# Performance work log

Measured on AMD Instinct MI355X. Metric: run time of the kernel, lower is better.

The kernel has to match this reference:

```python
import jax, jax.numpy as jnp
import numpy as np

B, S, D = 2, 2048, 1024
H = 16
HD = D // H  # 64


def _rope_tables(seq_len, head_dim, dtype=jnp.float32):
    inv_freq = 1.0 / (10000.0 ** (jnp.arange(0, head_dim, 2, dtype=jnp.float32) / head_dim))
    t = jnp.arange(seq_len, dtype=jnp.float32)
    freqs = jnp.einsum('i,j->ij', t, inv_freq)            # [S, HD/2]
    emb = jnp.concatenate([freqs, freqs], axis=-1)        # [S, HD]
    return jnp.cos(emb).astype(dtype)[None, None], jnp.sin(emb).astype(dtype)[None, None]


def _rotate_half(x):
    x1, x2 = x[..., : x.shape[-1] // 2], x[..., x.shape[-1] // 2 :]
    return jnp.concatenate([-x2, x1], axis=-1)


def setup_inputs() -> dict:
    key = jax.random.key(0)
    ks = jax.random.split(key, 9)
    s = 0.02
    return {
        'hidden_states': jax.random.normal(ks[0], (B, S, D), jnp.float32),
        'attention_mask': jnp.zeros((B, 1, S, S), jnp.float32),
        'Wq': jax.random.normal(ks[1], (D, D), jnp.float32) * s,
        'bq': jnp.zeros((D,), jnp.float32),
        'Wk': jax.random.normal(ks[2], (D, D), jnp.float32) * s,
        'bk': jnp.zeros((D,), jnp.float32),
        'Wv': jax.random.normal(ks[3], (D, D), jnp.float32) * s,
        'bv': jnp.zeros((D,), jnp.float32),
        'Wo': jax.random.normal(ks[4], (D, D), jnp.float32) * s,
        'bo': jnp.zeros((D,), jnp.float32),
    }


def reference(hidden_states, attention_mask, Wq, bq, Wk, bk, Wv, bv, Wo, bo):
    b, s = hidden_states.shape[:2]
    q = hidden_states @ Wq.T + bq
    k = hidden_states @ Wk.T + bk
    v = hidden_states @ Wv.T + bv
    # [B, H, S, HD]
    q = q.reshape(b, s, H, HD).transpose(0, 2, 1, 3)
    k = k.reshape(b, s, H, HD).transpose(0, 2, 1, 3)
    v = v.reshape(b, s, H, HD).transpose(0, 2, 1, 3)
    cos, sin = _rope_tables(s, HD, q.dtype)
    q = q * cos + _rotate_half(q) * sin
    k = k * cos + _rotate_half(k) * sin
    scaling = HD ** (-0.5)
    scores = jnp.einsum('bhqd,bhkd->bhqk', q, k) * scaling
    scores = scores / jnp.log(jnp.asarray(float(s), scores.dtype))  # dynamic NTK
    scores = scores + attention_mask
    probs = jax.nn.softmax(scores, axis=-1)
    out = jnp.einsum('bhqk,bhkd->bhqd', probs, v)
    out = out.transpose(0, 2, 1, 3).reshape(b, s, H * HD)
    return out @ Wo.T + bo
```

## Files before the change

### kernel.cpp

```cpp
#include <hip/hip_runtime.h>
#include <math.h>

#define S_LEN 2048
#define NHEAD 16
#define HDIM  64

typedef __attribute__((ext_vector_type(8))) short bf16x8;
typedef __attribute__((ext_vector_type(4))) float f32x4;

__device__ __forceinline__ unsigned short f2bf(float f) {
    union { float f; unsigned u; } v; v.f = f;
    unsigned r = v.u + 0x7fffu + ((v.u >> 16) & 1u);
    return (unsigned short)(r >> 16);
}

__device__ __forceinline__ void gl2lds16(const void* g, void* l) {
    __builtin_amdgcn_global_load_lds(
        (__attribute__((address_space(1))) void*)(void*)(g),
        (__attribute__((address_space(3))) void*)(l), 16, 0, 0);
}

__global__ __launch_bounds__(256) void convert_kernel(
    const float* __restrict__ hs, const float* __restrict__ Wq,
    const float* __restrict__ Wk, const float* __restrict__ Wv,
    const float* __restrict__ Wo, unsigned short* __restrict__ dst,
    float2* __restrict__ rtab)
{
    const int bid = blockIdx.x;
    if (bid >= 8192) {
        const int gid = (bid - 8192) * 256 + threadIdx.x;
        const int s = gid >> 5, i = gid & 31;
        const float l2c = 0.41524101186092029f;
        const float freq = exp2f(-(float)i * l2c);
        const float ang = (float)s * freq;
        float2 cs;
        cs.x = cosf(ang);
        cs.y = sinf(ang);
        rtab[gid] = cs;
        return;
    }
    const int gid = bid * 256 + threadIdx.x;
    const int n = gid << 2;
    const float* src; int off;
    if (n < (4 << 20))      { src = hs; off = n; }
    else if (n < (5 << 20)) { src = Wq; off = n - (4 << 20); }
    else if (n < (6 << 20)) { src = Wk; off = n - (5 << 20); }
    else if (n < (7 << 20)) { src = Wv; off = n - (6 << 20); }
    else                    { src = Wo; off = n - (7 << 20); }
    const float4 v = *(const float4*)(src + off);
    ushort4 o;
    o.x = f2bf(v.x); o.y = f2bf(v.y); o.z = f2bf(v.z); o.w = f2bf(v.w);
    *(ushort4*)(dst + n) = o;
}

__global__ __launch_bounds__(256, 3) void qkv_gemm_kernel(
    const unsigned short* __restrict__ X,
    const unsigned short* __restrict__ Wall,
    const float* __restrict__ bq, const float* __restrict__ bk,
    const float* __restrict__ bv, const float2* __restrict__ rtab,
    unsigned short* __restrict__ qo, unsigned short* __restrict__ ko,
    unsigned short* __restrict__ vo)
{
    __shared__ unsigned short As[128 * 64];
    __shared__ unsigned short Bs[128 * 64];

    const int mat = blockIdx.x >> 3;
    const int n0  = (blockIdx.x & 7) << 7;
    const int m0  = blockIdx.y << 7;
    const unsigned short* W = Wall + (mat << 20);
    const float* bias = (mat == 0) ? bq : (mat == 1) ? bk : bv;
    unsigned short* out = (mat == 0) ? qo : (mat == 1) ? ko : vo;

    const int tid = threadIdx.x;
    const int wave = tid >> 6, lane = tid & 63;
    const int quad = lane >> 4, ln = lane & 15;
    const int wm = (wave >> 1) << 6, wn = (wave & 1) << 6;

    const unsigned short* xptr[4];
    const unsigned short* wptr[4];
    #pragma unroll
    for (int L = 0; L < 4; ++L) {
        const int i = tid + (L << 8);
        const int r = i >> 3, cl = i & 7;
        const int cg = (cl ^ (r & 7)) << 3;
        const int rq = r & 63;
        const int tau = (mat < 2)
            ? ((r & 64) | ((rq & 15) << 1) | ((rq >> 4) & 1) | (((rq >> 5) & 1) << 5))
            : ((r & 64) | ((rq & 15) << 2) | (rq >> 4));
        xptr[L] = X + (m0 + r) * 1024 + cg;
        wptr[L] = W + (n0 + tau) * 1024 + cg;
    }

    f32x4 acc[4][4] = {};

    for (int k0 = 0; k0 < 1024; k0 += 64) {
        #pragma unroll
        for (int L = 0; L < 4; ++L) {
            const int i = tid + (L << 8);
            gl2lds16(xptr[L] + k0, &As[i << 3]);
            gl2lds16(wptr[L] + k0, &Bs[i << 3]);
        }
        __syncthreads();
        #pragma unroll
        for (int s = 0; s < 2; ++s) {
            bf16x8 a[4], b[4];
            #pragma unroll
            for (int t = 0; t < 4; ++t) {
                const int ra = wm + (t << 4) + ln;
                a[t] = *(const bf16x8*)&As[(ra << 6) + ((((s << 2) | quad) ^ (ra & 7)) << 3)];
                const int rb = wn + (t << 4) + ln;
                b[t] = *(const bf16x8*)&Bs[(rb << 6) + ((((s << 2) | quad) ^ (rb & 7)) << 3)];
            }
            #pragma unroll
            for (int i = 0; i < 4; ++i)
                #pragma unroll
                for (int j = 0; j < 4; ++j)
                    acc[i][j] = __builtin_amdgcn_mfma_f32_16x16x32_bf16(a[i], b[j], acc[i][j], 0, 0, 0);
        }
        __syncthreads();
    }

    const int h = (n0 + wn) >> 6;

    if (mat < 2) {
        const int nb = n0 + wn + (ln << 1);
        const float b0 = bias[nb],      b1 = bias[nb + 1];
        const float b2 = bias[nb + 32], b3 = bias[nb + 33];
        #pragma unroll
        for (int i = 0; i < 4; ++i) {
            #pragma unroll
            for (int reg = 0; reg < 4; ++reg) {
                const int m = m0 + wm + (i << 4) + (quad << 2) + reg;
                const int b_ = m >> 11, s_ = m & 2047;
                unsigned short* o = out + ((((b_ << 4) + h) << 11) + s_) * 64;
                const float4 cs = *(const float4*)(rtab + (s_ << 5) + (ln << 1));
                const float x1a = acc[i][0][reg] + b0, x1b = acc[i][1][reg] + b1;
                const float x2a = acc[i][2][reg] + b2, x2b = acc[i][3][reg] + b3;
                const float r0a = x1a * cs.x - x2a * cs.y;
                const float r0b = x1b * cs.z - x2b * cs.w;
                const float r1a = x2a * cs.x + x1a * cs.y;
                const float r1b = x2b * cs.z + x1b * cs.w;
                const unsigned ua = __float_as_uint(r0a) + 0x8000u;
                const unsigned ub = __float_as_uint(r0b) + 0x8000u;
                const unsigned uc = __float_as_uint(r1a) + 0x8000u;
                const unsigned ud = __float_as_uint(r1b) + 0x8000u;
                *(unsigned*)(o + (ln << 1))      = __builtin_amdgcn_perm(ub, ua, 0x07060302u);
                *(unsigned*)(o + 32 + (ln << 1)) = __builtin_amdgcn_perm(ud, uc, 0x07060302u);
            }
        }
    } else {
        const float4 bv4 = *(const float4*)(bias + n0 + wn + (ln << 2));
        #pragma unroll
        for (int i = 0; i < 4; ++i)
            #pragma unroll
            for (int reg = 0; reg < 4; ++reg) {
                const int m = m0 + wm + (i << 4) + (quad << 2) + reg;
                const int b_ = m >> 11, s_ = m & 2047;
                unsigned short* o = out + ((((b_ << 4) + h) << 11) + s_) * 64;
                const unsigned ua = __float_as_uint(acc[i][0][reg] + bv4.x) + 0x8000u;
                const unsigned ub = __float_as_uint(acc[i][1][reg] + bv4.y) + 0x8000u;
                const unsigned uc = __float_as_uint(acc[i][2][reg] + bv4.z) + 0x8000u;
                const unsigned ud = __float_as_uint(acc[i][3][reg] + bv4.w) + 0x8000u;
                uint2 w;
                w.x = __builtin_amdgcn_perm(ub, ua, 0x07060302u);
                w.y = __builtin_amdgcn_perm(ud, uc, 0x07060302u);
                *(uint2*)(o + (ln << 2)) = w;
            }
    }
}

__global__ __launch_bounds__(256) void vtrans_kernel(
    const unsigned short* __restrict__ v, unsigned short* __restrict__ vt)
{
    __shared__ unsigned short T[64][66];
    const int bh = blockIdx.x >> 5;
    const int s0 = (blockIdx.x & 31) << 6;
    const int tid = threadIdx.x;
    #pragma unroll
    for (int L = 0; L < 4; ++L) {
        const int i = tid + (L << 8);
        const int r = i >> 4, c4 = (i & 15) << 2;
        const ushort4 in = *(const ushort4*)(v + ((bh << 11) + s0 + r) * 64 + c4);
        T[r][c4 + 0] = in.x; T[r][c4 + 1] = in.y;
        T[r][c4 + 2] = in.z; T[r][c4 + 3] = in.w;
    }
    __syncthreads();
    #pragma unroll
    for (int L = 0; L < 4; ++L) {
        const int i = tid + (L << 8);
        const int hd = i >> 4, c4 = (i & 15) << 2;
        ushort4 o;
        o.x = T[c4 + 0][hd]; o.y = T[c4 + 1][hd];
        o.z = T[c4 + 2][hd]; o.w = T[c4 + 3][hd];
        *(ushort4*)(vt + ((bh << 6) + hd) * 2048 + s0 + c4) = o;
    }
}

__global__ __launch_bounds__(256, 4) void flash_kernel(
    const unsigned short* __restrict__ qb, const unsigned short* __restrict__ kb,
    const unsigned short* __restrict__ vtb, const float* __restrict__ mask,
    unsigned short* __restrict__ attn)
{
    __shared__ unsigned short Ks[2][64 * 64];
    __shared__ unsigned short Vt[2][64 * 64];
    __shared__ unsigned short Ps[64 * 64];

    const int qt = blockIdx.x & 31;
    const int bh = blockIdx.x >> 5;
    const int b_ = bh >> 4, h = bh & 15;
    const int q0 = qt << 6;

    const int tid = threadIdx.x;
    const int wave = tid >> 6, lane = tid & 63;
    const int quad = lane >> 4, ln = lane & 15;

    const unsigned short* qrow = qb + ((size_t)((bh << 11) + q0 + (wave << 4) + ln) << 6);
    bf16x8 qa[2];
    qa[0] = *(const bf16x8*)(qrow + (quad << 3));
    qa[1] = *(const bf16x8*)(qrow + 32 + (quad << 3));

    const float scale = 0.125f / logf(2048.0f);

    const float* mbase = mask + ((size_t)b_ << 22)
                       + ((size_t)(q0 + (wave << 4) + (quad << 2)) << 11) + (ln << 2);

    unsigned short* Pw = Ps + (wave << 10);

    const int i0 = tid, i1 = tid + 256;
    const int r0 = i0 >> 3, c0 = ((i0 & 7) ^ (r0 & 7)) << 3;
    const int r1 = i1 >> 3, c1 = ((i1 & 7) ^ (r1 & 7)) << 3;
    const int p0 = ((r0 & 15) << 2) + (r0 >> 4);
    const int p1 = ((r1 & 15) << 2) + (r1 >> 4);
    const unsigned short* kg0 = kb + ((bh << 11) + p0) * 64 + c0;
    const unsigned short* kg1 = kb + ((bh << 11) + p1) * 64 + c1;
    const unsigned short* vg0 = vtb + ((bh << 6) + r0) * 2048 + c0;
    const unsigned short* vg1 = vtb + ((bh << 6) + r1) * 2048 + c1;

    float l_i[4] = {0.f, 0.f, 0.f, 0.f};
    f32x4 O[4] = {};

    gl2lds16(kg0, &Ks[0][i0 << 3]);
    gl2lds16(kg1, &Ks[0][i1 << 3]);
    gl2lds16(vg0, &Vt[0][i0 << 3]);
    gl2lds16(vg1, &Vt[0][i1 << 3]);
    float4 mcur[4];
    #pragma unroll
    for (int reg = 0; reg < 4; ++reg)
        mcur[reg] = *(const float4*)(mbase + (reg << 11));

    for (int kt = 0; kt < 32; ++kt) {
        const int cur = kt & 1;

        __syncthreads();

        float4 mnext[4];
        if (kt < 31) {
            const int kn = (kt + 1) << 6;
            gl2lds16(kg0 + (kn << 6), &Ks[cur ^ 1][i0 << 3]);
            gl2lds16(kg1 + (kn << 6), &Ks[cur ^ 1][i1 << 3]);
            gl2lds16(vg0 + kn, &Vt[cur ^ 1][i0 << 3]);
            gl2lds16(vg1 + kn, &Vt[cur ^ 1][i1 << 3]);
            #pragma unroll
            for (int reg = 0; reg < 4; ++reg)
                mnext[reg] = *(const float4*)(mbase + kn + (reg << 11));
        }

        f32x4 sacc[4] = {};
        #pragma unroll
        for (int s = 0; s < 2; ++s) {
            bf16x8 bfr[4];
            #pragma unroll
            for (int j = 0; j < 4; ++j) {
                const int r = (j << 4) + ln;
                bfr[j] = *(const bf16x8*)&Ks[cur][(r << 6) + ((((s << 2) | quad) ^ (r & 7)) << 3)];
            }
            #pragma unroll
            for (int j = 0; j < 4; ++j)
                sacc[j] = __builtin_amdgcn_mfma_f32_16x16x32_bf16(qa[s], bfr[j], sacc[j], 0, 0, 0);
        }

        #pragma unroll
        for (int reg = 0; reg < 4; ++reg) {
            const int pr = (quad << 2) + reg;
            const float m0f = mcur[reg].x, m1f = mcur[reg].y,
                        m2f = mcur[reg].z, m3f = mcur[reg].w;
            float p[4];
            p[0] = __expf(fmaf(sacc[0][reg], scale, m0f));
            p[1] = __expf(fmaf(sacc[1][reg], scale, m1f));
            p[2] = __expf(fmaf(sacc[2][reg], scale, m2f));
            p[3] = __expf(fmaf(sacc[3][reg], scale, m3f));
            l_i[reg] += (p[0] + p[1]) + (p[2] + p[3]);
            unsigned u0 = __float_as_uint(p[0]) + 0x8000u;
            unsigned u1 = __float_as_uint(p[1]) + 0x8000u;
            unsigned u2 = __float_as_uint(p[2]) + 0x8000u;
            unsigned u3 = __float_as_uint(p[3]) + 0x8000u;
            uint2 w;
            w.x = __builtin_amdgcn_perm(u1, u0, 0x07060302u);
            w.y = __builtin_amdgcn_perm(u3, u2, 0x07060302u);
            const int e = (pr << 6) + ((((ln >> 1) ^ (pr & 7)) << 3)) + ((ln & 1) << 2);
            *(uint2*)&Pw[e] = w;
        }

        #pragma unroll
        for (int s = 0; s < 2; ++s) {
            const bf16x8 a = *(const bf16x8*)&Pw[(ln << 6) + ((((s << 2) | quad) ^ (ln & 7)) << 3)];
            bf16x8 bfr[4];
            #pragma unroll
            for (int j = 0; j < 4; ++j) {
                const int r = (j << 4) + ln;
                bfr[j] = *(const bf16x8*)&Vt[cur][(r << 6) + ((((s << 2) | quad) ^ (r & 7)) << 3)];
            }
            #pragma unroll
            for (int j = 0; j < 4; ++j)
                O[j] = __builtin_amdgcn_mfma_f32_16x16x32_bf16(a, bfr[j], O[j], 0, 0, 0);
        }

        if (kt < 31) {
            #pragma unroll
            for (int reg = 0; reg < 4; ++reg)
                mcur[reg] = mnext[reg];
        }
    }

    #pragma unroll
    for (int reg = 0; reg < 4; ++reg) {
        float l = l_i[reg];
        l += __shfl_xor(l, 1);
        l += __shfl_xor(l, 2);
        l += __shfl_xor(l, 4);
        l += __shfl_xor(l, 8);
        const float inv = 1.0f / l;
        const int qr = q0 + (wave << 4) + (quad << 2) + reg;
        unsigned short* op = attn + (((size_t)((b_ << 11) + qr)) << 10) + (h << 6);
        #pragma unroll
        for (int j = 0; j < 4; ++j)
            op[(j << 4) + ln] = f2bf(O[j][reg] * inv);
    }
}

__global__ __launch_bounds__(256, 3) void out_gemm_kernel(
    const unsigned short* __restrict__ X, const unsigned short* __restrict__ W,
    const float* __restrict__ bias, float* __restrict__ out)
{
    __shared__ unsigned short As[128 * 64];
    __shared__ unsigned short Bs[128 * 64];

    const int n0 = blockIdx.x << 7;
    const int m0 = blockIdx.y << 7;
    const int tid = threadIdx.x;
    const int wave = tid >> 6, lane = tid & 63;
    const int quad = lane >> 4, ln = lane & 15;
    const int wm = (wave >> 1) << 6, wn = (wave & 1) << 6;

    const unsigned short* xptr[4];
    const unsigned short* wptr[4];
    #pragma unroll
    for (int L = 0; L < 4; ++L) {
        const int i = tid + (L << 8);
        const int r = i >> 3, cl = i & 7;
        const int cg = (cl ^ (r & 7)) << 3;
        const int rq = r & 63;
        const int tau = (r & 64) | ((rq & 15) << 2) | (rq >> 4);
        xptr[L] = X + (m0 + r) * 1024 + cg;
        wptr[L] = W + (n0 + tau) * 1024 + cg;
    }

    f32x4 acc[4][4] = {};

    for (int k0 = 0; k0 < 1024; k0 += 64) {
        #pragma unroll
        for (int L = 0; L < 4; ++L) {
            const int i = tid + (L << 8);
            gl2lds16(xptr[L] + k0, &As[i << 3]);
            gl2lds16(wptr[L] + k0, &Bs[i << 3]);
        }
        __syncthreads();
        #pragma unroll
        for (int s = 0; s < 2; ++s) {
            bf16x8 a[4], b[4];
            #pragma unroll
            for (int t = 0; t < 4; ++t) {
                const int ra = wm + (t << 4) + ln;
                a[t] = *(const bf16x8*)&As[(ra << 6) + ((((s << 2) | quad) ^ (ra & 7)) << 3)];
                const int rb = wn + (t << 4) + ln;
                b[t] = *(const bf16x8*)&Bs[(rb << 6) + ((((s << 2) | quad) ^ (rb & 7)) << 3)];
            }
            #pragma unroll
            for (int i = 0; i < 4; ++i)
                #pragma unroll
                for (int j = 0; j < 4; ++j)
                    acc[i][j] = __builtin_amdgcn_mfma_f32_16x16x32_bf16(a[i], b[j], acc[i][j], 0, 0, 0);
        }
        __syncthreads();
    }

    const float4 bv4 = *(const float4*)(bias + n0 + wn + (ln << 2));

    #pragma unroll
    for (int i = 0; i < 4; ++i)
        #pragma unroll
        for (int reg = 0; reg < 4; ++reg) {
            const int m = m0 + wm + (i << 4) + (quad << 2) + reg;
            float4 ov;
            ov.x = acc[i][0][reg] + bv4.x;
            ov.y = acc[i][1][reg] + bv4.y;
            ov.z = acc[i][2][reg] + bv4.z;
            ov.w = acc[i][3][reg] + bv4.w;
            *(float4*)(out + m * 1024 + n0 + wn + (ln << 2)) = ov;
        }
}

extern "C" void kernel_launch(void* const* d_in, const int* in_sizes, int n_in,
                              void* d_out, int out_size, void* d_ws, size_t ws_size,
                              hipStream_t stream)
{
    const float* hs   = (const float*)d_in[0];
    const float* mask = (const float*)d_in[1];
    const float* Wq   = (const float*)d_in[2];
    const float* bq   = (const float*)d_in[3];
    const float* Wk   = (const float*)d_in[4];
    const float* bk   = (const float*)d_in[5];
    const float* Wv   = (const float*)d_in[6];
    const float* bv   = (const float*)d_in[7];
    const float* Wo   = (const float*)d_in[8];
    const float* bo   = (const float*)d_in[9];

    unsigned short* ws = (unsigned short*)d_ws;
    const size_t M1 = (size_t)1 << 20;
    unsigned short* hsb   = ws;
    unsigned short* wall  = ws + 4 * M1;
    unsigned short* wob   = ws + 7 * M1;
    unsigned short* qbf   = ws + 8 * M1;
    unsigned short* kbf   = ws + 12 * M1;
    unsigned short* vbf   = ws + 16 * M1;
    unsigned short* vtb   = ws + 20 * M1;
    unsigned short* attnb = ws + 24 * M1;
    float2*         rtab  = (float2*)(ws + 28 * M1);

    convert_kernel<<<8448, 256, 0, stream>>>(hs, Wq, Wk, Wv, Wo, ws, rtab);
    qkv_gemm_kernel<<<dim3(24, 32), 256, 0, stream>>>(hsb, wall, bq, bk, bv, rtab, qbf, kbf, vbf);
    vtrans_kernel<<<1024, 256, 0, stream>>>(vbf, vtb);
    flash_kernel<<<1024, 256, 0, stream>>>(qbf, kbf, vtb, mask, attnb);
    out_gemm_kernel<<<dim3(8, 32), 256, 0, stream>>>(attnb, wob, bo, (float*)d_out);
}
```

Measured before the change: 225.2 us.

## Fuse V transpose into QKV GEMM epilogue and software-pipeline PV in flash

The QKV GEMM epilogue for V now writes directly in transposed [bh, hd, s] layout, which removes the separate vtrans kernel launch and its extra global round trip. The flash kernel double-buffers the P tile in shared memory and defers each tile's P·V MFMA to the start of the next iteration, so it can overlap with the QK work, with a final PV step after the loop. In exchange, shared memory use grows and the launch bound drops to 3 blocks per CU, which may lower occupancy. The transposed V stores are 8-byte strided writes, which may coalesce less well.

```diff
diff --git a/kernel.cpp b/kernel.cpp
--- a/kernel.cpp
+++ b/kernel.cpp
@@ -59,7 +59,7 @@
     const float* __restrict__ bq, const float* __restrict__ bk,
     const float* __restrict__ bv, const float2* __restrict__ rtab,
     unsigned short* __restrict__ qo, unsigned short* __restrict__ ko,
-    unsigned short* __restrict__ vo)
+    unsigned short* __restrict__ vt)
 {
     __shared__ unsigned short As[128 * 64];
     __shared__ unsigned short Bs[128 * 64];
@@ -69,7 +69,6 @@
     const int m0  = blockIdx.y << 7;
     const unsigned short* W = Wall + (mat << 20);
     const float* bias = (mat == 0) ? bq : (mat == 1) ? bk : bv;
-    unsigned short* out = (mat == 0) ? qo : (mat == 1) ? ko : vo;
 
     const int tid = threadIdx.x;
     const int wave = tid >> 6, lane = tid & 63;
@@ -123,6 +122,7 @@
     const int h = (n0 + wn) >> 6;
 
     if (mat < 2) {
+        unsigned short* out = (mat == 0) ? qo : ko;
         const int nb = n0 + wn + (ln << 1);
         const float b0 = bias[nb],      b1 = bias[nb + 1];
         const float b2 = bias[nb + 32], b3 = bias[nb + 33];
@@ -150,60 +150,36 @@
         }
     } else {
         const float4 bv4 = *(const float4*)(bias + n0 + wn + (ln << 2));
-        #pragma unroll
-        for (int i = 0; i < 4; ++i)
-            #pragma unroll
-            for (int reg = 0; reg < 4; ++reg) {
-                const int m = m0 + wm + (i << 4) + (quad << 2) + reg;
-                const int b_ = m >> 11, s_ = m & 2047;
-                unsigned short* o = out + ((((b_ << 4) + h) << 11) + s_) * 64;
-                const unsigned ua = __float_as_uint(acc[i][0][reg] + bv4.x) + 0x8000u;
-                const unsigned ub = __float_as_uint(acc[i][1][reg] + bv4.y) + 0x8000u;
-                const unsigned uc = __float_as_uint(acc[i][2][reg] + bv4.z) + 0x8000u;
-                const unsigned ud = __float_as_uint(acc[i][3][reg] + bv4.w) + 0x8000u;
+        const float bvv[4] = {bv4.x, bv4.y, bv4.z, bv4.w};
+        #pragma unroll
+        for (int i = 0; i < 4; ++i) {
+            const int m = m0 + wm + (i << 4) + (quad << 2);
+            const int b_ = m >> 11, s_ = m & 2047;
+            const int bh = (b_ << 4) + h;
+            #pragma unroll
+            for (int jt = 0; jt < 4; ++jt) {
+                const int hd = (ln << 2) + jt;
+                const unsigned ua = __float_as_uint(acc[i][jt][0] + bvv[jt]) + 0x8000u;
+                const unsigned ub = __float_as_uint(acc[i][jt][1] + bvv[jt]) + 0x8000u;
+                const unsigned uc = __float_as_uint(acc[i][jt][2] + bvv[jt]) + 0x8000u;
+                const unsigned ud = __float_as_uint(acc[i][jt][3] + bvv[jt]) + 0x8000u;
                 uint2 w;
                 w.x = __builtin_amdgcn_perm(ub, ua, 0x07060302u);
                 w.y = __builtin_amdgcn_perm(ud, uc, 0x07060302u);
-                *(uint2*)(o + (ln << 2)) = w;
-            }
-    }
-}
-
-__global__ __launch_bounds__(256) void vtrans_kernel(
-    const unsigned short* __restrict__ v, unsigned short* __restrict__ vt)
-{
-    __shared__ unsigned short T[64][66];
-    const int bh = blockIdx.x >> 5;
-    const int s0 = (blockIdx.x & 31) << 6;
-    const int tid = threadIdx.x;
-    #pragma unroll
-    for (int L = 0; L < 4; ++L) {
-        const int i = tid + (L << 8);
-        const int r = i >> 4, c4 = (i & 15) << 2;
-        const ushort4 in = *(const ushort4*)(v + ((bh << 11) + s0 + r) * 64 + c4);
-        T[r][c4 + 0] = in.x; T[r][c4 + 1] = in.y;
-        T[r][c4 + 2] = in.z; T[r][c4 + 3] = in.w;
-    }
-    __syncthreads();
-    #pragma unroll
-    for (int L = 0; L < 4; ++L) {
-        const int i = tid + (L << 8);
-        const int hd = i >> 4, c4 = (i & 15) << 2;
-        ushort4 o;
-        o.x = T[c4 + 0][hd]; o.y = T[c4 + 1][hd];
-        o.z = T[c4 + 2][hd]; o.w = T[c4 + 3][hd];
-        *(ushort4*)(vt + ((bh << 6) + hd) * 2048 + s0 + c4) = o;
-    }
-}
-
-__global__ __launch_bounds__(256, 4) void flash_kernel(
+                *(uint2*)(vt + (((size_t)((bh << 6) + hd)) << 11) + s_) = w;
+            }
+        }
+    }
+}
+
+__global__ __launch_bounds__(256, 3) void flash_kernel(
     const unsigned short* __restrict__ qb, const unsigned short* __restrict__ kb,
     const unsigned short* __restrict__ vtb, const float* __restrict__ mask,
     unsigned short* __restrict__ attn)
 {
     __shared__ unsigned short Ks[2][64 * 64];
     __shared__ unsigned short Vt[2][64 * 64];
-    __shared__ unsigned short Ps[64 * 64];
+    __shared__ unsigned short Ps[2][64 * 64];
 
     const int qt = blockIdx.x & 31;
     const int bh = blockIdx.x >> 5;
@@ -224,7 +200,8 @@
     const float* mbase = mask + ((size_t)b_ << 22)
                        + ((size_t)(q0 + (wave << 4) + (quad << 2)) << 11) + (ln << 2);
 
-    unsigned short* Pw = Ps + (wave << 10);
+    unsigned short* Pw0 = Ps[0] + (wave << 10);
+    unsigned short* Pw1 = Ps[1] + (wave << 10);
 
     const int i0 = tid, i1 = tid + 256;
     const int r0 = i0 >> 3, c0 = ((i0 & 7) ^ (r0 & 7)) << 3;
@@ -251,6 +228,23 @@
     for (int kt = 0; kt < 32; ++kt) {
         const int cur = kt & 1;
 
+        if (kt > 0) {
+            const unsigned short* Pp = cur ? Pw0 : Pw1;
+            #pragma unroll
+            for (int s = 0; s < 2; ++s) {
+                const bf16x8 a = *(const bf16x8*)&Pp[(ln << 6) + ((((s << 2) | quad) ^ (ln & 7)) << 3)];
+                bf16x8 bfr[4];
+                #pragma unroll
+                for (int j = 0; j < 4; ++j) {
+                    const int r = (j << 4) + ln;
+                    bfr[j] = *(const bf16x8*)&Vt[cur ^ 1][(r << 6) + ((((s << 2) | quad) ^ (r & 7)) << 3)];
+                }
+                #pragma unroll
+                for (int j = 0; j < 4; ++j)
+                    O[j] = __builtin_amdgcn_mfma_f32_16x16x32_bf16(a, bfr[j], O[j], 0, 0, 0);
+            }
+        }
+
         __syncthreads();
 
         float4 mnext[4];
@@ -279,6 +273,7 @@
                 sacc[j] = __builtin_amdgcn_mfma_f32_16x16x32_bf16(qa[s], bfr[j], sacc[j], 0, 0, 0);
         }
 
+        unsigned short* Pw = cur ? Pw1 : Pw0;
         #pragma unroll
         for (int reg = 0; reg < 4; ++reg) {
             const int pr = (quad << 2) + reg;
@@ -301,25 +296,25 @@
             *(uint2*)&Pw[e] = w;
         }
 
-        #pragma unroll
-        for (int s = 0; s < 2; ++s) {
-            const bf16x8 a = *(const bf16x8*)&Pw[(ln << 6) + ((((s << 2) | quad) ^ (ln & 7)) << 3)];
-            bf16x8 bfr[4];
-            #pragma unroll
-            for (int j = 0; j < 4; ++j) {
-                const int r = (j << 4) + ln;
-                bfr[j] = *(const bf16x8*)&Vt[cur][(r << 6) + ((((s << 2) | quad) ^ (r & 7)) << 3)];
-            }
-            #pragma unroll
-            for (int j = 0; j < 4; ++j)
-                O[j] = __builtin_amdgcn_mfma_f32_16x16x32_bf16(a, bfr[j], O[j], 0, 0, 0);
-        }
-
         if (kt < 31) {
             #pragma unroll
             for (int reg = 0; reg < 4; ++reg)
                 mcur[reg] = mnext[reg];
         }
+    }
+
+    #pragma unroll
+    for (int s = 0; s < 2; ++s) {
+        const bf16x8 a = *(const bf16x8*)&Pw1[(ln << 6) + ((((s << 2) | quad) ^ (ln & 7)) << 3)];
+        bf16x8 bfr[4];
+        #pragma unroll
+        for (int j = 0; j < 4; ++j) {
+            const int r = (j << 4) + ln;
+            bfr[j] = *(const bf16x8*)&Vt[1][(r << 6) + ((((s << 2) | quad) ^ (r & 7)) << 3)];
+        }
+        #pragma unroll
+        for (int j = 0; j < 4; ++j)
+            O[j] = __builtin_amdgcn_mfma_f32_16x16x32_bf16(a, bfr[j], O[j], 0, 0, 0);
     }
 
     #pragma unroll
@@ -432,14 +427,12 @@
     unsigned short* wob   = ws + 7 * M1;
     unsigned short* qbf   = ws + 8 * M1;
     unsigned short* kbf   = ws + 12 * M1;
-    unsigned short* vbf   = ws + 16 * M1;
-    unsigned short* vtb   = ws + 20 * M1;
-    unsigned short* attnb = ws + 24 * M1;
-    float2*         rtab  = (float2*)(ws + 28 * M1);
+    unsigned short* vtb   = ws + 16 * M1;
+    unsigned short* attnb = ws + 20 * M1;
+    float2*         rtab  = (float2*)(ws + 24 * M1);
 
     convert_kernel<<<8448, 256, 0, stream>>>(hs, Wq, Wk, Wv, Wo, ws, rtab);
-    qkv_gemm_kernel<<<dim3(24, 32), 256, 0, stream>>>(hsb, wall, bq, bk, bv, rtab, qbf, kbf, vbf);
-    vtrans_kernel<<<1024, 256, 0, stream>>>(vbf, vtb);
+    qkv_gemm_kernel<<<dim3(24, 32), 256, 0, stream>>>(hsb, wall, bq, bk, bv, rtab, qbf, kbf, vtb);
     flash_kernel<<<1024, 256, 0, stream>>>(qbf, kbf, vtb, mask, attnb);
     out_gemm_kernel<<<dim3(8, 32), 256, 0, stream>>>(attnb, wob, bo, (float*)d_out);
 }
```

After: 248.5 us. +10.4%, slower.
